# Optimization experiments

Measured on AMD Instinct MI355X. Metric: run time of the kernel, lower is better.

The kernel has to match this reference:

```python
import jax, jax.numpy as jnp
import numpy as np

NUM_HEADS = 8
T = 8  # hardcoded temporal dim in the original forward
MD = 3  # max_displacement -> 7x7 window
EPS = 1e-12  # F.normalize eps


def l2_normalize(x, axis):
    n = jnp.sqrt(jnp.sum(x * x, axis=axis, keepdims=True))
    return x / jnp.maximum(n, EPS)


def correlation_7x7(q, k):
    # q, k: [B, C, H, W]; FlowNet-style correlation, kernel_size=1, max_disp=3.
    # out[b, u, v, h, w] = sum_c q[b,c,h,w] * k[b,c,h+u-3,w+v-3] (zero padded)
    B, C, H, W = q.shape
    kp = jnp.pad(k, ((0, 0), (0, 0), (MD, MD), (MD, MD)))
    outs = []
    for dy in range(2 * MD + 1):
        for dx in range(2 * MD + 1):
            ks = kp[:, :, dy:dy + H, dx:dx + W]
            outs.append(jnp.sum(q * ks, axis=1))  # [B, H, W]
    corr = jnp.stack(outs, axis=1)  # [B, 49, H, W]
    return corr.reshape(B, 2 * MD + 1, 2 * MD + 1, H, W)


def setup_inputs() -> dict:
    key = jax.random.key(0)
    ks = jax.random.split(key, 6)
    B, N, C = 8, 8192, 256
    hd = C // NUM_HEADS
    std = 0.02
    return {
        "x": jax.random.normal(ks[0], (B, N, C), dtype=jnp.float32),
        "w_qk": jax.random.normal(ks[1], (2 * C, C), dtype=jnp.float32) * std,
        "w_corr": jax.random.normal(ks[2], (hd, 49), dtype=jnp.float32) * std,
        "b_corr": jnp.zeros((hd,), dtype=jnp.float32),
        "w_proj": jax.random.normal(ks[3], (C, C), dtype=jnp.float32) * std,
        "b_proj": jnp.zeros((C,), dtype=jnp.float32),
    }


def reference(x, w_qk, w_corr, b_corr, w_proj, b_proj):
    B, N, C = x.shape
    nh = NUM_HEADS
    hd = C // nh
    H = int(np.sqrt(N // T))
    W = H

    # qk projection (no bias): [B, N, 2C] -> q, k each [B, nh, N, hd]
    qk = jnp.einsum('bnc,dc->bnd', x, w_qk)
    qk = qk.reshape(B, N, 2, nh, hd).transpose(2, 0, 3, 1, 4)
    q, k = qk[0], qk[1]

    # 'b n (t h w) d -> (b n) t d h w'
    q = q.reshape(B * nh, T, H, W, hd).transpose(0, 1, 4, 2, 3)
    k = k.reshape(B * nh, T, H, W, hd).transpose(0, 1, 4, 2, 3)

    # temporal postfix: k[t+1], last frame repeated
    k_post = jnp.concatenate([k[:, 1:], k[:, -1:]], axis=1)

    qp = q.reshape(B * nh * T, hd, H, W)
    kp = k_post.reshape(B * nh * T, hd, H, W)
    qp = l2_normalize(qp, axis=1)
    kp = l2_normalize(kp, axis=1)

    corr = correlation_7x7(qp, kp)  # [(B nh T), 7, 7, H, W]
    # 'b u v h w -> b (h w) (u v)'
    corr = corr.transpose(0, 3, 4, 1, 2).reshape(B * nh * T, H * W, 49)

    v = jnp.einsum('bpk,dk->bpd', corr, w_corr) + b_corr  # [(B nh T), HW, hd]

    # '(b n t) (h w) d -> b n (t h w) d' then 'b h n d -> b n (h d)'
    out = v.reshape(B, nh, T * H * W, hd).transpose(0, 2, 1, 3).reshape(B, N, C)
    out = jnp.einsum('bnc,dc->bnd', out, w_proj) + b_proj
    return out
```

## Files before the change

### kernel.cpp

```cpp
#include <hip/hip_runtime.h>

typedef _Float16 half8 __attribute__((ext_vector_type(8)));
typedef _Float16 half2v __attribute__((ext_vector_type(2)));
typedef float float4v __attribute__((ext_vector_type(4)));

__device__ __forceinline__ float dot2acc(unsigned a, unsigned b, float c) {
#if __has_builtin(__builtin_amdgcn_fdot2)
  return __builtin_amdgcn_fdot2(__builtin_bit_cast(half2v, a), __builtin_bit_cast(half2v, b), c, false);
#else
  half2v ha = __builtin_bit_cast(half2v, a);
  half2v hb = __builtin_bit_cast(half2v, b);
  c += (float)ha[0] * (float)hb[0];
  c += (float)ha[1] * (float)hb[1];
  return c;
#endif
}
__device__ __forceinline__ unsigned pack2(float a, float b) {
  half2v h;
  h[0] = (_Float16)a;
  h[1] = (_Float16)b;
  return __builtin_bit_cast(unsigned, h);
}
__device__ __forceinline__ void gload_lds16(const void* g, void* l) {
  __builtin_amdgcn_global_load_lds((const __attribute__((address_space(1))) unsigned*)g,
                                   (__attribute__((address_space(3))) unsigned*)l, 16, 0, 0);
}

__global__ void cvt_w(const float4* __restrict__ wqk, const float4* __restrict__ wpj,
                      ushort4* __restrict__ wqk16, ushort4* __restrict__ wpj16) {
  int b = blockIdx.x;
  const float4* s;
  ushort4* d;
  int i;
  if (b < 128) { s = wqk; d = wqk16; i = b * 256 + threadIdx.x; }
  else { s = wpj; d = wpj16; i = (b - 128) * 256 + threadIdx.x; }
  float4 v = s[i];
  _Float16 a = (_Float16)v.x, bb = (_Float16)v.y, c = (_Float16)v.z, e = (_Float16)v.w;
  ushort4 o;
  o.x = __builtin_bit_cast(unsigned short, a);
  o.y = __builtin_bit_cast(unsigned short, bb);
  o.z = __builtin_bit_cast(unsigned short, c);
  o.w = __builtin_bit_cast(unsigned short, e);
  d[i] = o;
}

__global__ __launch_bounds__(512, 4)
void gemm_qk(const float* __restrict__ X, const _Float16* __restrict__ Bw,
             _Float16* __restrict__ qo, _Float16* __restrict__ ko) {
  __shared__ _Float16 Ash[2][4096];
  __shared__ _Float16 Bsh[2][8192];
  const int tid = threadIdx.x;
  const int lane = tid & 63, w = tid >> 6;
  const int wm = w >> 2, wn = w & 3;
  const int ml = lane & 15, qd = lane >> 4;
  const int m0 = blockIdx.y * 128, n0 = blockIdx.x * 256;

  float4v acc[4][4];
  float4v z = {0.f, 0.f, 0.f, 0.f};
#pragma unroll
  for (int i = 0; i < 4; ++i)
#pragma unroll
    for (int j = 0; j < 4; ++j) acc[i][j] = z;

  const float* Xp = X + (size_t)m0 * 256;
  const _Float16* Bp = Bw + (size_t)n0 * 256;
  const int ar = tid >> 2, aj = tid & 3;
  const int ajx = aj ^ ((ar >> 1) & 3);
  const int rB0 = tid >> 2, jB0 = (tid & 3) ^ ((rB0 >> 1) & 3);
  const int rB1 = (tid + 512) >> 2, jB1 = (tid & 3) ^ ((rB1 >> 1) & 3);

  float4 a0 = *(const float4*)(Xp + (size_t)ar * 256 + ajx * 8);
  float4 a1 = *(const float4*)(Xp + (size_t)ar * 256 + ajx * 8 + 4);
  gload_lds16(Bp + rB0 * 256 + jB0 * 8, &Bsh[0][(size_t)(w * 64) * 8]);
  gload_lds16(Bp + rB1 * 256 + jB1 * 8, &Bsh[0][(size_t)(512 + w * 64) * 8]);
  {
    half8 h;
    h[0] = (_Float16)a0.x; h[1] = (_Float16)a0.y; h[2] = (_Float16)a0.z; h[3] = (_Float16)a0.w;
    h[4] = (_Float16)a1.x; h[5] = (_Float16)a1.y; h[6] = (_Float16)a1.z; h[7] = (_Float16)a1.w;
    *(half8*)(&Ash[0][ar * 32 + aj * 8]) = h;
  }
  __syncthreads();

#pragma unroll
  for (int kt = 0; kt < 8; ++kt) {
    const int cur = kt & 1;
    float4 n0f, n1f;
    if (kt < 7) {
      const int k0 = (kt + 1) * 32;
      n0f = *(const float4*)(Xp + (size_t)ar * 256 + k0 + ajx * 8);
      n1f = *(const float4*)(Xp + (size_t)ar * 256 + k0 + ajx * 8 + 4);
      gload_lds16(Bp + rB0 * 256 + k0 + jB0 * 8, &Bsh[cur ^ 1][(size_t)(w * 64) * 8]);
      gload_lds16(Bp + rB1 * 256 + k0 + jB1 * 8, &Bsh[cur ^ 1][(size_t)(512 + w * 64) * 8]);
    }
    half8 af[4], bf[4];
#pragma unroll
    for (int im = 0; im < 4; ++im) {
      int rr = wm * 64 + im * 16 + ml;
      af[im] = *(const half8*)(&Ash[cur][rr * 32 + (qd ^ ((rr >> 1) & 3)) * 8]);
      int rc = wn * 64 + im * 16 + ml;
      bf[im] = *(const half8*)(&Bsh[cur][rc * 32 + (qd ^ ((rc >> 1) & 3)) * 8]);
    }
#pragma unroll
    for (int im = 0; im < 4; ++im)
#pragma unroll
      for (int in = 0; in < 4; ++in)
        acc[im][in] = __builtin_amdgcn_mfma_f32_16x16x32_f16(bf[in], af[im], acc[im][in], 0, 0, 0);
    if (kt < 7) {
      half8 h;
      h[0] = (_Float16)n0f.x; h[1] = (_Float16)n0f.y; h[2] = (_Float16)n0f.z; h[3] = (_Float16)n0f.w;
      h[4] = (_Float16)n1f.x; h[5] = (_Float16)n1f.y; h[6] = (_Float16)n1f.z; h[7] = (_Float16)n1f.w;
      *(half8*)(&Ash[cur ^ 1][ar * 32 + aj * 8]) = h;
    }
    __syncthreads();
  }

#pragma unroll
  for (int im = 0; im < 4; ++im) {
    int rowr = m0 + wm * 64 + im * 16 + ml;
    int b = rowr >> 13, n = rowr & 8191;
    int t = n >> 10, yx = n & 1023;
#pragma unroll
    for (int hh = 0; hh < 2; ++hh) {
      float ss = 0.f;
#pragma unroll
      for (int ii = 0; ii < 2; ++ii) {
        int in = hh * 2 + ii;
#pragma unroll
        for (int r = 0; r < 4; ++r) ss += acc[im][in][r] * acc[im][in][r];
      }
      ss += __shfl_xor(ss, 16);
      ss += __shfl_xor(ss, 32);
      float sc = 1.f / fmaxf(sqrtf(ss), 1e-12f);
#pragma unroll
      for (int ii = 0; ii < 2; ++ii) {
        int in = hh * 2 + ii;
        int col = n0 + wn * 64 + in * 16 + qd * 4;
        int s = col >> 8, h = (col >> 5) & 7, j = col & 31;
        _Float16* dst = s ? ko : qo;
        int p = b * 64 + h * 8 + t;
        uint2 pk;
        pk.x = pack2(acc[im][in][0] * sc, acc[im][in][1] * sc);
        pk.y = pack2(acc[im][in][2] * sc, acc[im][in][3] * sc);
        *(uint2*)(dst + ((size_t)p * 1024 + yx) * 32 + j) = pk;
      }
    }
  }
}

__global__ __launch_bounds__(256, 4)
void corr_kernel(const _Float16* __restrict__ q16, const _Float16* __restrict__ k16,
                 const float* __restrict__ wcorr, const float* __restrict__ bcorr,
                 _Float16* __restrict__ outp) {
  __shared__ uint4 smem[2304];
  __shared__ uint4 wcs[256];

  const int tid = threadIdx.x;
  const int bx = blockIdx.x;
  const int p = bx >> 2, tile = bx & 3;
  const int y0 = (tile >> 1) * 16, x0 = (tile & 1) * 16;
  const int b = p >> 6, h = (p >> 3) & 7, t = p & 7;
  const int pk = (t < 7) ? p + 1 : p;
  const int ty = tid >> 4, tx = tid & 15;

  _Float16* wch = (_Float16*)wcs;
  for (int idx = tid; idx < 2048; idx += 256) {
    int d = idx >> 6, kk = idx & 63;
    float v = (kk < 49) ? wcorr[d * 49 + kk] : (kk == 49 ? bcorr[d] : 0.f);
    wch[idx] = (_Float16)v;
  }

  const _Float16* kbase = k16 + (size_t)pk * 32768;
#pragma unroll
  for (int i = 0; i < 8; ++i) {
    int g = tid + i * 256;
    if (g < 1936) {
      int vec = g >> 2, part = g & 3;
      int ky = vec / 22, kx = vec - ky * 22;
      int gy = y0 + ky - 3, gx = x0 + kx - 3;
      uint4 val = make_uint4(0u, 0u, 0u, 0u);
      if (gy >= 0 && gy < 32 && gx >= 0 && gx < 32)
        val = *(const uint4*)(kbase + ((size_t)gy * 32 + gx) * 32 + part * 8);
      int slot = (vec << 2) | (part ^ (vec & 3) ^ ((vec >> 2) & 3));
      smem[slot] = val;
    }
  }

  const _Float16* qptr = q16 + (size_t)p * 32768 + ((size_t)(y0 + ty) * 32 + (x0 + tx)) * 32;
  uint4 qv[4];
#pragma unroll
  for (int i = 0; i < 4; ++i) qv[i] = *(const uint4*)(qptr + i * 8);
  unsigned* qu = (unsigned*)qv;
  __syncthreads();

  float corr[49];
#pragma unroll
  for (int dy = 0; dy < 7; ++dy) {
#pragma unroll
    for (int dx = 0; dx < 7; ++dx) {
      int vec = (ty + dy) * 22 + (tx + dx);
      int base = vec << 2;
      int sw = (vec & 3) ^ ((vec >> 2) & 3);
      float c = 0.f;
#pragma unroll
      for (int pq = 0; pq < 4; ++pq) {
        uint4 kk = smem[base | (pq ^ sw)];
        const unsigned* ku = (const unsigned*)&kk;
#pragma unroll
        for (int e = 0; e < 4; ++e) c = dot2acc(qu[pq * 4 + e], ku[e], c);
      }
      corr[dy * 7 + dx] = c;
    }
  }
  __syncthreads();

#pragma unroll
  for (int i = 0; i < 8; ++i) {
    uint4 val;
    unsigned* vu = (unsigned*)&val;
#pragma unroll
    for (int e = 0; e < 4; ++e) {
      int idx = i * 8 + e * 2;
      half2v hh;
      hh[0] = (_Float16)(idx < 49 ? corr[idx] : (idx == 49 ? 1.f : 0.f));
      hh[1] = (_Float16)(idx + 1 < 49 ? corr[idx + 1] : (idx + 1 == 49 ? 1.f : 0.f));
      vu[e] = __builtin_bit_cast(unsigned, hh);
    }
    smem[tid * 9 + i] = val;
  }
  __syncthreads();

  _Float16* corrm = (_Float16*)smem;
  const int lane = tid & 63, w = tid >> 6;
  const int ml = lane & 15, qd = lane >> 4;
  float4v vacc[4][2];
  float4v z = {0.f, 0.f, 0.f, 0.f};
#pragma unroll
  for (int im = 0; im < 4; ++im) { vacc[im][0] = z; vacc[im][1] = z; }
#pragma unroll
  for (int ks = 0; ks < 2; ++ks) {
    half8 bfrag[2];
#pragma unroll
    for (int nt = 0; nt < 2; ++nt)
      bfrag[nt] = *(const half8*)(wch + (nt * 16 + ml) * 64 + ks * 32 + qd * 8);
#pragma unroll
    for (int im = 0; im < 4; ++im) {
      half8 afrag = *(const half8*)(corrm + (w * 64 + im * 16 + ml) * 72 + ks * 32 + qd * 8);
#pragma unroll
      for (int nt = 0; nt < 2; ++nt)
        vacc[im][nt] = __builtin_amdgcn_mfma_f32_16x16x32_f16(afrag, bfrag[nt], vacc[im][nt], 0, 0, 0);
    }
  }

#pragma unroll
  for (int im = 0; im < 4; ++im) {
#pragma unroll
    for (int nt = 0; nt < 2; ++nt) {
      int d = nt * 16 + ml;
#pragma unroll
      for (int r = 0; r < 4; ++r) {
        int pos = w * 64 + im * 16 + qd * 4 + r;
        int py = pos >> 4, px = pos & 15;
        int n = t * 1024 + (y0 + py) * 32 + (x0 + px);
        outp[(((size_t)b * 8192 + n) << 8) + h * 32 + d] = (_Float16)vacc[im][nt][r];
      }
    }
  }
}

__global__ __launch_bounds__(512, 4)
void gemm_proj(const _Float16* __restrict__ A, const _Float16* __restrict__ Bw,
               const float* __restrict__ bp, float* __restrict__ out) {
  __shared__ _Float16 Ash[2][4096];
  __shared__ _Float16 Bsh[2][8192];
  const int tid = threadIdx.x;
  const int lane = tid & 63, w = tid >> 6;
  const int wm = w >> 2, wn = w & 3;
  const int ml = lane & 15, qd = lane >> 4;
  const int m0 = blockIdx.x * 128;

  float4v acc[4][4];
  float4v z = {0.f, 0.f, 0.f, 0.f};
#pragma unroll
  for (int i = 0; i < 4; ++i)
#pragma unroll
    for (int j = 0; j < 4; ++j) acc[i][j] = z;

  const _Float16* Ap = A + (size_t)m0 * 256;
  const _Float16* Bp = Bw;
  const int rA = tid >> 2, jA = (tid & 3) ^ ((rA >> 1) & 3);
  const int rB1 = (tid + 512) >> 2, jB1 = (tid & 3) ^ ((rB1 >> 1) & 3);

  gload_lds16(Ap + rA * 256 + jA * 8, &Ash[0][(size_t)(w * 64) * 8]);
  gload_lds16(Bp + rA * 256 + jA * 8, &Bsh[0][(size_t)(w * 64) * 8]);
  gload_lds16(Bp + rB1 * 256 + jB1 * 8, &Bsh[0][(size_t)(512 + w * 64) * 8]);
  __syncthreads();

#pragma unroll
  for (int kt = 0; kt < 8; ++kt) {
    const int cur = kt & 1;
    if (kt < 7) {
      const int k0 = (kt + 1) * 32;
      const int nb = cur ^ 1;
      gload_lds16(Ap + rA * 256 + k0 + jA * 8, &Ash[nb][(size_t)(w * 64) * 8]);
      gload_lds16(Bp + rA * 256 + k0 + jA * 8, &Bsh[nb][(size_t)(w * 64) * 8]);
      gload_lds16(Bp + rB1 * 256 + k0 + jB1 * 8, &Bsh[nb][(size_t)(512 + w * 64) * 8]);
    }
    half8 af[4], bf[4];
#pragma unroll
    for (int im = 0; im < 4; ++im) {
      int rr = wm * 64 + im * 16 + ml;
      af[im] = *(const half8*)(&Ash[cur][rr * 32 + (qd ^ ((rr >> 1) & 3)) * 8]);
      int rc = wn * 64 + im * 16 + ml;
      bf[im] = *(const half8*)(&Bsh[cur][rc * 32 + (qd ^ ((rc >> 1) & 3)) * 8]);
    }
#pragma unroll
    for (int im = 0; im < 4; ++im)
#pragma unroll
      for (int in = 0; in < 4; ++in)
        acc[im][in] = __builtin_amdgcn_mfma_f32_16x16x32_f16(bf[in], af[im], acc[im][in], 0, 0, 0);
    __syncthreads();
  }

#pragma unroll
  for (int im = 0; im < 4; ++im) {
    int rowr = m0 + wm * 64 + im * 16 + ml;
#pragma unroll
    for (int in = 0; in < 4; ++in) {
      int col = wn * 64 + in * 16 + qd * 4;
      float4 bb = *(const float4*)(bp + col);
      float4 o;
      o.x = acc[im][in][0] + bb.x;
      o.y = acc[im][in][1] + bb.y;
      o.z = acc[im][in][2] + bb.z;
      o.w = acc[im][in][3] + bb.w;
      *(float4*)(out + (size_t)rowr * 256 + col) = o;
    }
  }
}

extern "C" void kernel_launch(void* const* d_in, const int* in_sizes, int n_in,
                              void* d_out, int out_size, void* d_ws, size_t ws_size,
                              hipStream_t stream) {
  const float* x      = (const float*)d_in[0];
  const float* w_qk   = (const float*)d_in[1];
  const float* w_corr = (const float*)d_in[2];
  const float* b_corr = (const float*)d_in[3];
  const float* w_proj = (const float*)d_in[4];
  const float* b_proj = (const float*)d_in[5];
  float* out = (float*)d_out;

  char* ws = (char*)d_ws;
  _Float16* q16   = (_Float16*)(ws + 33554432);
  _Float16* k16   = (_Float16*)(ws + 67108864);
  _Float16* op16  = (_Float16*)(ws + 100663296);
  _Float16* wqk16 = (_Float16*)(ws + 134217728);
  _Float16* wpj16 = (_Float16*)(ws + 134479872);

  cvt_w<<<192, 256, 0, stream>>>((const float4*)w_qk, (const float4*)w_proj,
                                 (ushort4*)wqk16, (ushort4*)wpj16);
  gemm_qk<<<dim3(2, 512), 512, 0, stream>>>(x, wqk16, q16, k16);
  corr_kernel<<<2048, 256, 0, stream>>>(q16, k16, w_corr, b_corr, op16);
  gemm_proj<<<512, 512, 0, stream>>>(op16, wpj16, b_proj, out);
}
```

Baseline: 215.4 us.

## Deepen GEMM A-operand prefetch with explicit waitcnt scheduling and block swizzle

Both GEMM kernels now prefetch the A operand two k-steps ahead into registers while B goes one step ahead through direct global-to-LDS loads. Plain __syncthreads is replaced by explicit vmcnt/lgkmcnt waits, sched_barriers and s_barrier, so global loads stay in flight across the MFMA block. gemm_proj moves A from direct-to-LDS loads to register staging. gemm_qk also gets a 1D grid with a block-index swizzle that places the two N-halves of an M tile close together in launch order for L2 reuse of X. The hand-written waitcnt counts depend on exact instruction ordering and may be wrong if the compiler reorders loads, and the extra register buffers raise register pressure.

```diff
diff --git a/kernel.cpp b/kernel.cpp
--- a/kernel.cpp
+++ b/kernel.cpp
@@ -24,6 +24,16 @@
 __device__ __forceinline__ void gload_lds16(const void* g, void* l) {
   __builtin_amdgcn_global_load_lds((const __attribute__((address_space(1))) unsigned*)g,
                                    (__attribute__((address_space(3))) unsigned*)l, 16, 0, 0);
+}
+__device__ __forceinline__ void sbar0() { __builtin_amdgcn_sched_barrier(0); }
+#define WAITVM(n) asm volatile("s_waitcnt vmcnt(" #n ")" ::: "memory")
+#define WAITLGKM asm volatile("s_waitcnt lgkmcnt(0)" ::: "memory")
+
+__device__ __forceinline__ void cvt_store8(_Float16* dst, float4 a, float4 b) {
+  half8 h;
+  h[0] = (_Float16)a.x; h[1] = (_Float16)a.y; h[2] = (_Float16)a.z; h[3] = (_Float16)a.w;
+  h[4] = (_Float16)b.x; h[5] = (_Float16)b.y; h[6] = (_Float16)b.z; h[7] = (_Float16)b.w;
+  *(half8*)dst = h;
 }
 
 __global__ void cvt_w(const float4* __restrict__ wqk, const float4* __restrict__ wpj,
@@ -53,7 +63,10 @@
   const int lane = tid & 63, w = tid >> 6;
   const int wm = w >> 2, wn = w & 3;
   const int ml = lane & 15, qd = lane >> 4;
-  const int m0 = blockIdx.y * 128, n0 = blockIdx.x * 256;
+  const int bid = blockIdx.x;
+  const int yb = ((bid >> 4) << 3) | (bid & 7);
+  const int xb = (bid >> 3) & 1;
+  const int m0 = yb * 128, n0 = xb * 256;
 
   float4v acc[4][4];
   float4v z = {0.f, 0.f, 0.f, 0.f};
@@ -67,31 +80,35 @@
   const int ar = tid >> 2, aj = tid & 3;
   const int ajx = aj ^ ((ar >> 1) & 3);
   const int rB0 = tid >> 2, jB0 = (tid & 3) ^ ((rB0 >> 1) & 3);
-  const int rB1 = (tid + 512) >> 2, jB1 = (tid & 3) ^ ((rB1 >> 1) & 3);
-
-  float4 a0 = *(const float4*)(Xp + (size_t)ar * 256 + ajx * 8);
-  float4 a1 = *(const float4*)(Xp + (size_t)ar * 256 + ajx * 8 + 4);
+  const int rB1 = rB0 + 128, jB1 = (tid & 3) ^ ((rB1 >> 1) & 3);
+
+  float4 xs[2][2];
   gload_lds16(Bp + rB0 * 256 + jB0 * 8, &Bsh[0][(size_t)(w * 64) * 8]);
   gload_lds16(Bp + rB1 * 256 + jB1 * 8, &Bsh[0][(size_t)(512 + w * 64) * 8]);
-  {
-    half8 h;
-    h[0] = (_Float16)a0.x; h[1] = (_Float16)a0.y; h[2] = (_Float16)a0.z; h[3] = (_Float16)a0.w;
-    h[4] = (_Float16)a1.x; h[5] = (_Float16)a1.y; h[6] = (_Float16)a1.z; h[7] = (_Float16)a1.w;
-    *(half8*)(&Ash[0][ar * 32 + aj * 8]) = h;
-  }
-  __syncthreads();
+  sbar0();
+  xs[0][0] = *(const float4*)(Xp + (size_t)ar * 256 + ajx * 8);
+  xs[0][1] = *(const float4*)(Xp + (size_t)ar * 256 + ajx * 8 + 4);
+  sbar0();
+  xs[1][0] = *(const float4*)(Xp + (size_t)ar * 256 + 32 + ajx * 8);
+  xs[1][1] = *(const float4*)(Xp + (size_t)ar * 256 + 32 + ajx * 8 + 4);
+  WAITVM(2);
+  sbar0();
+  cvt_store8(&Ash[0][ar * 32 + aj * 8], xs[0][0], xs[0][1]);
+  WAITLGKM;
+  sbar0();
+  __builtin_amdgcn_s_barrier();
+  sbar0();
 
 #pragma unroll
   for (int kt = 0; kt < 8; ++kt) {
-    const int cur = kt & 1;
-    float4 n0f, n1f;
-    if (kt < 7) {
-      const int k0 = (kt + 1) * 32;
-      n0f = *(const float4*)(Xp + (size_t)ar * 256 + k0 + ajx * 8);
-      n1f = *(const float4*)(Xp + (size_t)ar * 256 + k0 + ajx * 8 + 4);
-      gload_lds16(Bp + rB0 * 256 + k0 + jB0 * 8, &Bsh[cur ^ 1][(size_t)(w * 64) * 8]);
-      gload_lds16(Bp + rB1 * 256 + k0 + jB1 * 8, &Bsh[cur ^ 1][(size_t)(512 + w * 64) * 8]);
-    }
+    const int cur = kt & 1, nbuf = cur ^ 1;
+    const int kB = (kt + 1 < 8 ? kt + 1 : 7) * 32;
+    const int kX = (kt + 2 < 8 ? kt + 2 : 7) * 32;
+    gload_lds16(Bp + rB0 * 256 + kB + jB0 * 8, &Bsh[nbuf][(size_t)(w * 64) * 8]);
+    gload_lds16(Bp + rB1 * 256 + kB + jB1 * 8, &Bsh[nbuf][(size_t)(512 + w * 64) * 8]);
+    sbar0();
+    xs[kt & 1][0] = *(const float4*)(Xp + (size_t)ar * 256 + kX + ajx * 8);
+    xs[kt & 1][1] = *(const float4*)(Xp + (size_t)ar * 256 + kX + ajx * 8 + 4);
     half8 af[4], bf[4];
 #pragma unroll
     for (int im = 0; im < 4; ++im) {
@@ -105,13 +122,13 @@
 #pragma unroll
       for (int in = 0; in < 4; ++in)
         acc[im][in] = __builtin_amdgcn_mfma_f32_16x16x32_f16(bf[in], af[im], acc[im][in], 0, 0, 0);
-    if (kt < 7) {
-      half8 h;
-      h[0] = (_Float16)n0f.x; h[1] = (_Float16)n0f.y; h[2] = (_Float16)n0f.z; h[3] = (_Float16)n0f.w;
-      h[4] = (_Float16)n1f.x; h[5] = (_Float16)n1f.y; h[6] = (_Float16)n1f.z; h[7] = (_Float16)n1f.w;
-      *(half8*)(&Ash[cur ^ 1][ar * 32 + aj * 8]) = h;
-    }
-    __syncthreads();
+    WAITVM(2);
+    sbar0();
+    cvt_store8(&Ash[nbuf][ar * 32 + aj * 8], xs[(kt + 1) & 1][0], xs[(kt + 1) & 1][1]);
+    WAITLGKM;
+    sbar0();
+    __builtin_amdgcn_s_barrier();
+    sbar0();
   }
 
 #pragma unroll
@@ -287,24 +304,35 @@
 
   const _Float16* Ap = A + (size_t)m0 * 256;
   const _Float16* Bp = Bw;
-  const int rA = tid >> 2, jA = (tid & 3) ^ ((rA >> 1) & 3);
-  const int rB1 = (tid + 512) >> 2, jB1 = (tid & 3) ^ ((rB1 >> 1) & 3);
-
-  gload_lds16(Ap + rA * 256 + jA * 8, &Ash[0][(size_t)(w * 64) * 8]);
-  gload_lds16(Bp + rA * 256 + jA * 8, &Bsh[0][(size_t)(w * 64) * 8]);
+  const int ar = tid >> 2, aj = tid & 3;
+  const int ajx = aj ^ ((ar >> 1) & 3);
+  const int rB0 = tid >> 2, jB0 = (tid & 3) ^ ((rB0 >> 1) & 3);
+  const int rB1 = rB0 + 128, jB1 = (tid & 3) ^ ((rB1 >> 1) & 3);
+
+  uint4 as[2];
+  gload_lds16(Bp + rB0 * 256 + jB0 * 8, &Bsh[0][(size_t)(w * 64) * 8]);
   gload_lds16(Bp + rB1 * 256 + jB1 * 8, &Bsh[0][(size_t)(512 + w * 64) * 8]);
-  __syncthreads();
+  sbar0();
+  as[0] = *(const uint4*)(Ap + (size_t)ar * 256 + ajx * 8);
+  sbar0();
+  as[1] = *(const uint4*)(Ap + (size_t)ar * 256 + 32 + ajx * 8);
+  WAITVM(1);
+  sbar0();
+  *(uint4*)(&Ash[0][ar * 32 + aj * 8]) = as[0];
+  WAITLGKM;
+  sbar0();
+  __builtin_amdgcn_s_barrier();
+  sbar0();
 
 #pragma unroll
   for (int kt = 0; kt < 8; ++kt) {
-    const int cur = kt & 1;
-    if (kt < 7) {
-      const int k0 = (kt + 1) * 32;
-      const int nb = cur ^ 1;
-      gload_lds16(Ap + rA * 256 + k0 + jA * 8, &Ash[nb][(size_t)(w * 64) * 8]);
-      gload_lds16(Bp + rA * 256 + k0 + jA * 8, &Bsh[nb][(size_t)(w * 64) * 8]);
-      gload_lds16(Bp + rB1 * 256 + k0 + jB1 * 8, &Bsh[nb][(size_t)(512 + w * 64) * 8]);
-    }
+    const int cur = kt & 1, nbuf = cur ^ 1;
+    const int kB = (kt + 1 < 8 ? kt + 1 : 7) * 32;
+    const int kA = (kt + 2 < 8 ? kt + 2 : 7) * 32;
+    gload_lds16(Bp + rB0 * 256 + kB + jB0 * 8, &Bsh[nbuf][(size_t)(w * 64) * 8]);
+    gload_lds16(Bp + rB1 * 256 + kB + jB1 * 8, &Bsh[nbuf][(size_t)(512 + w * 64) * 8]);
+    sbar0();
+    as[kt & 1] = *(const uint4*)(Ap + (size_t)ar * 256 + kA + ajx * 8);
     half8 af[4], bf[4];
 #pragma unroll
     for (int im = 0; im < 4; ++im) {
@@ -318,7 +346,13 @@
 #pragma unroll
       for (int in = 0; in < 4; ++in)
         acc[im][in] = __builtin_amdgcn_mfma_f32_16x16x32_f16(bf[in], af[im], acc[im][in], 0, 0, 0);
-    __syncthreads();
+    WAITVM(1);
+    sbar0();
+    *(uint4*)(&Ash[nbuf][ar * 32 + aj * 8]) = as[(kt + 1) & 1];
+    WAITLGKM;
+    sbar0();
+    __builtin_amdgcn_s_barrier();
+    sbar0();
   }
 
 #pragma unroll
@@ -358,7 +392,7 @@
 
   cvt_w<<<192, 256, 0, stream>>>((const float4*)w_qk, (const float4*)w_proj,
                                  (ushort4*)wqk16, (ushort4*)wpj16);
-  gemm_qk<<<dim3(2, 512), 512, 0, stream>>>(x, wqk16, q16, k16);
+  gemm_qk<<<1024, 512, 0, stream>>>(x, wqk16, q16, k16);
   corr_kernel<<<2048, 256, 0, stream>>>(q16, k16, w_corr, b_corr, op16);
   gemm_proj<<<512, 512, 0, stream>>>(op16, wpj16, b_proj, out);
 }
```

After: 217.0 us. No clear change (+0.7%).
